# Kernel optimization log

Measured on AMD Instinct MI355X. Metric: run time of the kernel, lower is better.

Reference implementation:

```python
import jax, jax.numpy as jnp
import numpy as np


def setup_inputs() -> dict:
    key = jax.random.key(0)
    k1, k2 = jax.random.split(key)
    qs = jax.random.normal(k1, (64, 32, 128), dtype=jnp.float32)   # (n_queries, n_query_tokens, dim)
    ps = jax.random.normal(k2, (64, 1024, 128), dtype=jnp.float32)  # (n_docs, n_doc_tokens, dim)
    return {"qs": qs, "ps": ps}


def reference(qs, ps):
    # ColBERT MaxSim: for each (query b, doc c), sum over query tokens of the
    # max similarity against all doc tokens.
    # scores[b,c,n,s] = sum_d qs[b,n,d] * ps[c,s,d]
    sim = jnp.einsum('bnd,csd->bcns', qs, ps)  # (n_q, n_d, tok_q, tok_d)
    scores = sim.max(axis=3).sum(axis=2)       # (n_q, n_d)
    return scores
```

## Files before the change

### kernel.cpp

```cpp
#include <hip/hip_runtime.h>
#include <stdint.h>


typedef __bf16 bf16x8 __attribute__((ext_vector_type(8)));
typedef float floatx16 __attribute__((ext_vector_type(16)));

#define QS_N (64u * 32u * 128u)
#define PS_N (64u * 1024u * 128u)

__device__ inline unsigned short f2bf(float f) {
  union { float f; uint32_t u; } x{f};
  uint32_t r = (x.u + 0x7FFFu + ((x.u >> 16) & 1u)) >> 16;
  return (unsigned short)r;
}

__global__ __launch_bounds__(256) void cvt_kernel(const float* __restrict__ qs,
                                                  const float* __restrict__ ps,
                                                  ushort* __restrict__ outb) {
  const int nq4 = QS_N / 4;
  const int n4 = (QS_N + PS_N) / 4;
  int i = blockIdx.x * 256 + threadIdx.x;
  if (i >= n4) return;
  float4 f;
  if (i < nq4) {
    f = ((const float4*)qs)[i];
  } else {
    f = ((const float4*)ps)[i - nq4];
  }
  ushort4 o;
  o.x = f2bf(f.x); o.y = f2bf(f.y); o.z = f2bf(f.z); o.w = f2bf(f.w);
  ((ushort4*)outb)[i] = o;
}

union FragU { uint4 u; bf16x8 v; };

__device__ inline bf16x8 load_frag_bf16(const ushort* p) {
  FragU f;
  f.u = *(const uint4*)p;
  return f.v;
}

__device__ inline bf16x8 load_frag_f32(const float* p) {
  float4 a = *(const float4*)p;
  float4 b = *(const float4*)(p + 4);
  union { ushort s[8]; bf16x8 v; } r;
  r.s[0] = f2bf(a.x); r.s[1] = f2bf(a.y); r.s[2] = f2bf(a.z); r.s[3] = f2bf(a.w);
  r.s[4] = f2bf(b.x); r.s[5] = f2bf(b.y); r.s[6] = f2bf(b.z); r.s[7] = f2bf(b.w);
  return r.v;
}

template <bool PRECVT>
__device__ inline bf16x8 load_a(const void* p, int off) {
  return PRECVT ? load_frag_bf16((const ushort*)p + off)
                : load_frag_f32((const float*)p + off);
}

template <bool PRECVT>
__global__ __launch_bounds__(256) void maxsim_kernel(const void* __restrict__ qsv,
                                                     const void* __restrict__ psv,
                                                     float* __restrict__ out) {
  const int lane = threadIdx.x & 63;
  const int wave = threadIdx.x >> 6;

  const int xcd = blockIdx.x & 7;
  const int slot = blockIdx.x >> 3;
  const int c = xcd * 8 + (slot >> 4);
  const int bg = slot & 15;
  const int row = lane & 31;
  const int koff = (lane >> 5) * 8;
  const int b0 = bg * 4;

  const int pbase = (c * 1024 + wave * 256 + row) * 128 + koff;

  bf16x8 a0[8], a1[8];
#pragma unroll
  for (int k = 0; k < 8; ++k) a0[k] = load_a<PRECVT>(psv, pbase + k * 16);

  bf16x8 qf[4][8];
#pragma unroll
  for (int b = 0; b < 4; ++b)
#pragma unroll
    for (int k = 0; k < 8; ++k)
      qf[b][k] = load_a<PRECVT>(qsv, ((b0 + b) * 32 + row) * 128 + k * 16 + koff);

  float vmax[4];
#pragma unroll
  for (int b = 0; b < 4; ++b) vmax[b] = -3.4e38f;

#pragma unroll 1
  for (int t = 0; t < 8; t += 2) {
#pragma unroll
    for (int k = 0; k < 8; ++k)
      a1[k] = load_a<PRECVT>(psv, pbase + (t + 1) * 4096 + k * 16);
#pragma unroll
    for (int b = 0; b < 4; ++b) {
      floatx16 acc = {0, 0, 0, 0, 0, 0, 0, 0, 0, 0, 0, 0, 0, 0, 0, 0};
#pragma unroll
      for (int k = 0; k < 8; ++k)
        acc = __builtin_amdgcn_mfma_f32_32x32x16_bf16(a0[k], qf[b][k], acc, 0, 0, 0);
      float m0 = fmaxf(fmaxf(fmaxf(acc[0], acc[1]), fmaxf(acc[2], acc[3])),
                       fmaxf(fmaxf(acc[4], acc[5]), fmaxf(acc[6], acc[7])));
      float m1 = fmaxf(fmaxf(fmaxf(acc[8], acc[9]), fmaxf(acc[10], acc[11])),
                       fmaxf(fmaxf(acc[12], acc[13]), fmaxf(acc[14], acc[15])));
      vmax[b] = fmaxf(vmax[b], fmaxf(m0, m1));
    }
    int t2 = t + 2;
    if (t2 > 7) t2 = 0;
#pragma unroll
    for (int k = 0; k < 8; ++k)
      a0[k] = load_a<PRECVT>(psv, pbase + t2 * 4096 + k * 16);
#pragma unroll
    for (int b = 0; b < 4; ++b) {
      floatx16 acc = {0, 0, 0, 0, 0, 0, 0, 0, 0, 0, 0, 0, 0, 0, 0, 0};
#pragma unroll
      for (int k = 0; k < 8; ++k)
        acc = __builtin_amdgcn_mfma_f32_32x32x16_bf16(a1[k], qf[b][k], acc, 0, 0, 0);
      float m0 = fmaxf(fmaxf(fmaxf(acc[0], acc[1]), fmaxf(acc[2], acc[3])),
                       fmaxf(fmaxf(acc[4], acc[5]), fmaxf(acc[6], acc[7])));
      float m1 = fmaxf(fmaxf(fmaxf(acc[8], acc[9]), fmaxf(acc[10], acc[11])),
                       fmaxf(fmaxf(acc[12], acc[13]), fmaxf(acc[14], acc[15])));
      vmax[b] = fmaxf(vmax[b], fmaxf(m0, m1));
    }
  }

#pragma unroll
  for (int b = 0; b < 4; ++b) vmax[b] = fmaxf(vmax[b], __shfl_xor(vmax[b], 32, 64));

  __shared__ float red[4][4][32];
  if (lane < 32) {
#pragma unroll
    for (int b = 0; b < 4; ++b) red[wave][b][lane] = vmax[b];
  }
  __syncthreads();
  if (threadIdx.x < 128) {
    const int b = threadIdx.x >> 5;
    const int n = threadIdx.x & 31;
    float m = fmaxf(fmaxf(red[0][b][n], red[1][b][n]), fmaxf(red[2][b][n], red[3][b][n]));
#pragma unroll
    for (int o = 16; o > 0; o >>= 1) m += __shfl_xor(m, o, 32);
    if (n == 0) out[(b0 + b) * 64 + c] = m;
  }
}

extern "C" void kernel_launch(void* const* d_in, const int* in_sizes, int n_in,
                              void* d_out, int out_size, void* d_ws, size_t ws_size,
                              hipStream_t stream) {
  const float* qs = (const float*)d_in[0];
  const float* ps = (const float*)d_in[1];
  float* out = (float*)d_out;

  const size_t need = (QS_N + PS_N) * sizeof(ushort);

  if (ws_size >= need) {
    ushort* wsb = (ushort*)d_ws;
    const int n4 = (int)((QS_N + PS_N) / 4);
    cvt_kernel<<<(n4 + 255) / 256, 256, 0, stream>>>(qs, ps, wsb);
    maxsim_kernel<true><<<dim3(64 * 16), dim3(256), 0, stream>>>(wsb, wsb + QS_N, out);
  } else {
    maxsim_kernel<false><<<dim3(64 * 16), dim3(256), 0, stream>>>(qs, ps, out);
  }
}
```

Baseline: 129.2 us.

## Stage query fragments in LDS and interleave four independent MFMA accumulators

Query fragments are now loaded cooperatively into shared memory once per block and read from LDS inside the loop, instead of each wave holding all 32 query fragments in registers. The MFMA loop is reordered so four independent accumulator chains run interleaved over k, which hides MFMA dependency latency. This frees many VGPRs, which can raise occupancy, at the cost of repeated LDS reads and a block-wide barrier at the start.

```diff
diff --git a/kernel.cpp b/kernel.cpp
--- a/kernel.cpp
+++ b/kernel.cpp
@@ -55,6 +55,16 @@
                 : load_frag_f32((const float*)p + off);
 }
 
+__device__ inline float rmax16(const floatx16& a) {
+  float m0 = fmaxf(fmaxf(a[0], a[1]), fmaxf(a[2], a[3]));
+  float m1 = fmaxf(fmaxf(a[4], a[5]), fmaxf(a[6], a[7]));
+  float m2 = fmaxf(fmaxf(a[8], a[9]), fmaxf(a[10], a[11]));
+  float m3 = fmaxf(fmaxf(a[12], a[13]), fmaxf(a[14], a[15]));
+  return fmaxf(fmaxf(m0, m1), fmaxf(m2, m3));
+}
+
+#define ZERO16 {0, 0, 0, 0, 0, 0, 0, 0, 0, 0, 0, 0, 0, 0, 0, 0}
+
 template <bool PRECVT>
 __global__ __launch_bounds__(256) void maxsim_kernel(const void* __restrict__ qsv,
                                                      const void* __restrict__ psv,
@@ -66,22 +76,44 @@
   const int slot = blockIdx.x >> 3;
   const int c = xcd * 8 + (slot >> 4);
   const int bg = slot & 15;
+  const int b0 = bg * 4;
   const int row = lane & 31;
   const int koff = (lane >> 5) * 8;
-  const int b0 = bg * 4;
+
+  __shared__ ushort lds_q[4 * 8 * 64 * 8];
+  {
+    uint4* dst = (uint4*)lds_q;
+#pragma unroll
+    for (int i = 0; i < 8; ++i) {
+      const int id = threadIdx.x + i * 256;
+      const int l = id & 63;
+      const int k = (id >> 6) & 7;
+      const int b = id >> 9;
+      const int goff = ((b0 + b) * 32 + (l & 31)) * 128 + k * 16 + (l >> 5) * 8;
+      uint4 v;
+      if (PRECVT) {
+        v = *(const uint4*)((const ushort*)qsv + goff);
+      } else {
+        const float* q = (const float*)qsv + goff;
+        float4 x = *(const float4*)q;
+        float4 y = *(const float4*)(q + 4);
+        union { ushort s[8]; uint4 u; } r;
+        r.s[0] = f2bf(x.x); r.s[1] = f2bf(x.y); r.s[2] = f2bf(x.z); r.s[3] = f2bf(x.w);
+        r.s[4] = f2bf(y.x); r.s[5] = f2bf(y.y); r.s[6] = f2bf(y.z); r.s[7] = f2bf(y.w);
+        v = r.u;
+      }
+      dst[id] = v;
+    }
+  }
+  __syncthreads();
+
+  const ushort* lq = lds_q + lane * 8;
 
   const int pbase = (c * 1024 + wave * 256 + row) * 128 + koff;
 
   bf16x8 a0[8], a1[8];
 #pragma unroll
   for (int k = 0; k < 8; ++k) a0[k] = load_a<PRECVT>(psv, pbase + k * 16);
-
-  bf16x8 qf[4][8];
-#pragma unroll
-  for (int b = 0; b < 4; ++b)
-#pragma unroll
-    for (int k = 0; k < 8; ++k)
-      qf[b][k] = load_a<PRECVT>(qsv, ((b0 + b) * 32 + row) * 128 + k * 16 + koff);
 
   float vmax[4];
 #pragma unroll
@@ -92,34 +124,46 @@
 #pragma unroll
     for (int k = 0; k < 8; ++k)
       a1[k] = load_a<PRECVT>(psv, pbase + (t + 1) * 4096 + k * 16);
-#pragma unroll
-    for (int b = 0; b < 4; ++b) {
-      floatx16 acc = {0, 0, 0, 0, 0, 0, 0, 0, 0, 0, 0, 0, 0, 0, 0, 0};
-#pragma unroll
-      for (int k = 0; k < 8; ++k)
-        acc = __builtin_amdgcn_mfma_f32_32x32x16_bf16(a0[k], qf[b][k], acc, 0, 0, 0);
-      float m0 = fmaxf(fmaxf(fmaxf(acc[0], acc[1]), fmaxf(acc[2], acc[3])),
-                       fmaxf(fmaxf(acc[4], acc[5]), fmaxf(acc[6], acc[7])));
-      float m1 = fmaxf(fmaxf(fmaxf(acc[8], acc[9]), fmaxf(acc[10], acc[11])),
-                       fmaxf(fmaxf(acc[12], acc[13]), fmaxf(acc[14], acc[15])));
-      vmax[b] = fmaxf(vmax[b], fmaxf(m0, m1));
+    {
+      floatx16 acc0 = ZERO16, acc1 = ZERO16, acc2 = ZERO16, acc3 = ZERO16;
+#pragma unroll
+      for (int k = 0; k < 8; ++k) {
+        bf16x8 q0 = *(const bf16x8*)(lq + (0 * 8 + k) * 512);
+        bf16x8 q1 = *(const bf16x8*)(lq + (1 * 8 + k) * 512);
+        bf16x8 q2 = *(const bf16x8*)(lq + (2 * 8 + k) * 512);
+        bf16x8 q3 = *(const bf16x8*)(lq + (3 * 8 + k) * 512);
+        acc0 = __builtin_amdgcn_mfma_f32_32x32x16_bf16(a0[k], q0, acc0, 0, 0, 0);
+        acc1 = __builtin_amdgcn_mfma_f32_32x32x16_bf16(a0[k], q1, acc1, 0, 0, 0);
+        acc2 = __builtin_amdgcn_mfma_f32_32x32x16_bf16(a0[k], q2, acc2, 0, 0, 0);
+        acc3 = __builtin_amdgcn_mfma_f32_32x32x16_bf16(a0[k], q3, acc3, 0, 0, 0);
+      }
+      vmax[0] = fmaxf(vmax[0], rmax16(acc0));
+      vmax[1] = fmaxf(vmax[1], rmax16(acc1));
+      vmax[2] = fmaxf(vmax[2], rmax16(acc2));
+      vmax[3] = fmaxf(vmax[3], rmax16(acc3));
     }
     int t2 = t + 2;
     if (t2 > 7) t2 = 0;
 #pragma unroll
     for (int k = 0; k < 8; ++k)
       a0[k] = load_a<PRECVT>(psv, pbase + t2 * 4096 + k * 16);
-#pragma unroll
-    for (int b = 0; b < 4; ++b) {
-      floatx16 acc = {0, 0, 0, 0, 0, 0, 0, 0, 0, 0, 0, 0, 0, 0, 0, 0};
-#pragma unroll
-      for (int k = 0; k < 8; ++k)
-        acc = __builtin_amdgcn_mfma_f32_32x32x16_bf16(a1[k], qf[b][k], acc, 0, 0, 0);
-      float m0 = fmaxf(fmaxf(fmaxf(acc[0], acc[1]), fmaxf(acc[2], acc[3])),
-                       fmaxf(fmaxf(acc[4], acc[5]), fmaxf(acc[6], acc[7])));
-      float m1 = fmaxf(fmaxf(fmaxf(acc[8], acc[9]), fmaxf(acc[10], acc[11])),
-                       fmaxf(fmaxf(acc[12], acc[13]), fmaxf(acc[14], acc[15])));
-      vmax[b] = fmaxf(vmax[b], fmaxf(m0, m1));
+    {
+      floatx16 acc0 = ZERO16, acc1 = ZERO16, acc2 = ZERO16, acc3 = ZERO16;
+#pragma unroll
+      for (int k = 0; k < 8; ++k) {
+        bf16x8 q0 = *(const bf16x8*)(lq + (0 * 8 + k) * 512);
+        bf16x8 q1 = *(const bf16x8*)(lq + (1 * 8 + k) * 512);
+        bf16x8 q2 = *(const bf16x8*)(lq + (2 * 8 + k) * 512);
+        bf16x8 q3 = *(const bf16x8*)(lq + (3 * 8 + k) * 512);
+        acc0 = __builtin_amdgcn_mfma_f32_32x32x16_bf16(a1[k], q0, acc0, 0, 0, 0);
+        acc1 = __builtin_amdgcn_mfma_f32_32x32x16_bf16(a1[k], q1, acc1, 0, 0, 0);
+        acc2 = __builtin_amdgcn_mfma_f32_32x32x16_bf16(a1[k], q2, acc2, 0, 0, 0);
+        acc3 = __builtin_amdgcn_mfma_f32_32x32x16_bf16(a1[k], q3, acc3, 0, 0, 0);
+      }
+      vmax[0] = fmaxf(vmax[0], rmax16(acc0));
+      vmax[1] = fmaxf(vmax[1], rmax16(acc1));
+      vmax[2] = fmaxf(vmax[2], rmax16(acc2));
+      vmax[3] = fmaxf(vmax[3], rmax16(acc3));
     }
   }
 
```

After: 135.0 us. 4.5% more time.

## Switch MaxSim MFMA tiles from 32x32x16 to 16x16x32 with smaller register footprint

Applied to the files above, without the earlier changes.

Replaces the 32x32x16 bf16 MFMA tiling with 16x16x32 MFMAs. Each wave now processes 16 doc rows per step over 16 steps, and query fragments are split into two 16-row halves. Accumulators shrink from 16 floats to 4 per tile, and launch_bounds now requests 2 blocks per CU, aiming for higher occupancy and better latency hiding. The cost is more MFMA instructions per tile, more shuffle reductions, and an empty asm barrier that pins the query registers.

```diff
diff --git a/kernel.cpp b/kernel.cpp
--- a/kernel.cpp
+++ b/kernel.cpp
@@ -3,7 +3,7 @@
 
 
 typedef __bf16 bf16x8 __attribute__((ext_vector_type(8)));
-typedef float floatx16 __attribute__((ext_vector_type(16)));
+typedef float floatx4 __attribute__((ext_vector_type(4)));
 
 #define QS_N (64u * 32u * 128u)
 #define PS_N (64u * 1024u * 128u)
@@ -34,31 +34,54 @@
 
 union FragU { uint4 u; bf16x8 v; };
 
-__device__ inline bf16x8 load_frag_bf16(const ushort* p) {
-  FragU f;
-  f.u = *(const uint4*)p;
-  return f.v;
-}
-
-__device__ inline bf16x8 load_frag_f32(const float* p) {
-  float4 a = *(const float4*)p;
-  float4 b = *(const float4*)(p + 4);
-  union { ushort s[8]; bf16x8 v; } r;
-  r.s[0] = f2bf(a.x); r.s[1] = f2bf(a.y); r.s[2] = f2bf(a.z); r.s[3] = f2bf(a.w);
-  r.s[4] = f2bf(b.x); r.s[5] = f2bf(b.y); r.s[6] = f2bf(b.z); r.s[7] = f2bf(b.w);
-  return r.v;
+__device__ inline bf16x8 as_frag(uint4 u) {
+  FragU x;
+  x.u = u;
+  return x.v;
 }
 
 template <bool PRECVT>
-__device__ inline bf16x8 load_a(const void* p, int off) {
-  return PRECVT ? load_frag_bf16((const ushort*)p + off)
-                : load_frag_f32((const float*)p + off);
+__device__ inline uint4 load16(const void* p, int off) {
+  if (PRECVT) {
+    return *(const uint4*)((const ushort*)p + off);
+  } else {
+    const float* q = (const float*)p + off;
+    float4 x = *(const float4*)q;
+    float4 y = *(const float4*)(q + 4);
+    union { ushort s[8]; uint4 u; } r;
+    r.s[0] = f2bf(x.x); r.s[1] = f2bf(x.y); r.s[2] = f2bf(x.z); r.s[3] = f2bf(x.w);
+    r.s[4] = f2bf(y.x); r.s[5] = f2bf(y.y); r.s[6] = f2bf(y.z); r.s[7] = f2bf(y.w);
+    return r.u;
+  }
 }
 
+#define ZERO4 {0, 0, 0, 0}
+
+#define TILE_COMPUTE(ABUF)                                                      \
+  {                                                                             \
+    floatx4 acc[4][2];                                                          \
+    _Pragma("unroll") for (int b = 0; b < 4; ++b)                               \
+      _Pragma("unroll") for (int h = 0; h < 2; ++h)                             \
+        acc[b][h] = (floatx4)ZERO4;                                             \
+    _Pragma("unroll") for (int k2 = 0; k2 < 4; ++k2) {                          \
+      bf16x8 af = as_frag(ABUF[k2]);                                            \
+      _Pragma("unroll") for (int b = 0; b < 4; ++b)                             \
+        _Pragma("unroll") for (int h = 0; h < 2; ++h)                           \
+          acc[b][h] = __builtin_amdgcn_mfma_f32_16x16x32_bf16(                  \
+              af, as_frag(qfr[b][h][k2]), acc[b][h], 0, 0, 0);                  \
+    }                                                                           \
+    _Pragma("unroll") for (int b = 0; b < 4; ++b)                               \
+      _Pragma("unroll") for (int h = 0; h < 2; ++h) {                           \
+        float m = fmaxf(fmaxf(acc[b][h][0], acc[b][h][1]),                      \
+                        fmaxf(acc[b][h][2], acc[b][h][3]));                     \
+        vmax[b][h] = fmaxf(vmax[b][h], m);                                      \
+      }                                                                         \
+  }
+
 template <bool PRECVT>
-__global__ __launch_bounds__(256) void maxsim_kernel(const void* __restrict__ qsv,
-                                                     const void* __restrict__ psv,
-                                                     float* __restrict__ out) {
+__global__ __launch_bounds__(256, 2) void maxsim_kernel(const void* __restrict__ qsv,
+                                                        const void* __restrict__ psv,
+                                                        float* __restrict__ out) {
   const int lane = threadIdx.x & 63;
   const int wave = threadIdx.x >> 6;
 
@@ -66,70 +89,68 @@
   const int slot = blockIdx.x >> 3;
   const int c = xcd * 8 + (slot >> 4);
   const int bg = slot & 15;
-  const int row = lane & 31;
-  const int koff = (lane >> 5) * 8;
   const int b0 = bg * 4;
 
-  const int pbase = (c * 1024 + wave * 256 + row) * 128 + koff;
+  const int idx16 = lane & 15;
+  const int koff = (lane >> 4) * 8;
 
-  bf16x8 a0[8], a1[8];
-#pragma unroll
-  for (int k = 0; k < 8; ++k) a0[k] = load_a<PRECVT>(psv, pbase + k * 16);
-
-  bf16x8 qf[4][8];
+  uint4 qfr[4][2][4];
 #pragma unroll
   for (int b = 0; b < 4; ++b)
 #pragma unroll
-    for (int k = 0; k < 8; ++k)
-      qf[b][k] = load_a<PRECVT>(qsv, ((b0 + b) * 32 + row) * 128 + k * 16 + koff);
+    for (int h = 0; h < 2; ++h)
+#pragma unroll
+      for (int k2 = 0; k2 < 4; ++k2) {
+        const int goff = ((b0 + b) * 32 + h * 16 + idx16) * 128 + k2 * 32 + koff;
+        uint4 v = load16<PRECVT>(qsv, goff);
+        asm volatile("" : "+v"(v.x), "+v"(v.y), "+v"(v.z), "+v"(v.w));
+        qfr[b][h][k2] = v;
+      }
 
-  float vmax[4];
+  const int pbase = (c * 1024 + wave * 256 + idx16) * 128 + koff;
+
+  uint4 a0[4], a1[4];
 #pragma unroll
-  for (int b = 0; b < 4; ++b) vmax[b] = -3.4e38f;
+  for (int k2 = 0; k2 < 4; ++k2) a0[k2] = load16<PRECVT>(psv, pbase + k2 * 32);
+
+  float vmax[4][2];
+#pragma unroll
+  for (int b = 0; b < 4; ++b) {
+    vmax[b][0] = -3.4e38f;
+    vmax[b][1] = -3.4e38f;
+  }
 
 #pragma unroll 1
-  for (int t = 0; t < 8; t += 2) {
+  for (int t = 0; t < 16; t += 2) {
 #pragma unroll
-    for (int k = 0; k < 8; ++k)
-      a1[k] = load_a<PRECVT>(psv, pbase + (t + 1) * 4096 + k * 16);
+    for (int k2 = 0; k2 < 4; ++k2)
+      a1[k2] = load16<PRECVT>(psv, pbase + (t + 1) * 2048 + k2 * 32);
+    TILE_COMPUTE(a0)
+    int t2 = t + 2;
+    if (t2 > 15) t2 = 0;
 #pragma unroll
-    for (int b = 0; b < 4; ++b) {
-      floatx16 acc = {0, 0, 0, 0, 0, 0, 0, 0, 0, 0, 0, 0, 0, 0, 0, 0};
-#pragma unroll
-      for (int k = 0; k < 8; ++k)
-        acc = __builtin_amdgcn_mfma_f32_32x32x16_bf16(a0[k], qf[b][k], acc, 0, 0, 0);
-      float m0 = fmaxf(fmaxf(fmaxf(acc[0], acc[1]), fmaxf(acc[2], acc[3])),
-                       fmaxf(fmaxf(acc[4], acc[5]), fmaxf(acc[6], acc[7])));
-      float m1 = fmaxf(fmaxf(fmaxf(acc[8], acc[9]), fmaxf(acc[10], acc[11])),
-                       fmaxf(fmaxf(acc[12], acc[13]), fmaxf(acc[14], acc[15])));
-      vmax[b] = fmaxf(vmax[b], fmaxf(m0, m1));
-    }
-    int t2 = t + 2;
-    if (t2 > 7) t2 = 0;
-#pragma unroll
-    for (int k = 0; k < 8; ++k)
-      a0[k] = load_a<PRECVT>(psv, pbase + t2 * 4096 + k * 16);
-#pragma unroll
-    for (int b = 0; b < 4; ++b) {
-      floatx16 acc = {0, 0, 0, 0, 0, 0, 0, 0, 0, 0, 0, 0, 0, 0, 0, 0};
-#pragma unroll
-      for (int k = 0; k < 8; ++k)
-        acc = __builtin_amdgcn_mfma_f32_32x32x16_bf16(a1[k], qf[b][k], acc, 0, 0, 0);
-      float m0 = fmaxf(fmaxf(fmaxf(acc[0], acc[1]), fmaxf(acc[2], acc[3])),
-                       fmaxf(fmaxf(acc[4], acc[5]), fmaxf(acc[6], acc[7])));
-      float m1 = fmaxf(fmaxf(fmaxf(acc[8], acc[9]), fmaxf(acc[10], acc[11])),
-                       fmaxf(fmaxf(acc[12], acc[13]), fmaxf(acc[14], acc[15])));
-      vmax[b] = fmaxf(vmax[b], fmaxf(m0, m1));
-    }
+    for (int k2 = 0; k2 < 4; ++k2)
+      a0[k2] = load16<PRECVT>(psv, pbase + t2 * 2048 + k2 * 32);
+    TILE_COMPUTE(a1)
   }
 
 #pragma unroll
-  for (int b = 0; b < 4; ++b) vmax[b] = fmaxf(vmax[b], __shfl_xor(vmax[b], 32, 64));
+  for (int b = 0; b < 4; ++b)
+#pragma unroll
+    for (int h = 0; h < 2; ++h) {
+      float v = vmax[b][h];
+      v = fmaxf(v, __shfl_xor(v, 16, 64));
+      v = fmaxf(v, __shfl_xor(v, 32, 64));
+      vmax[b][h] = v;
+    }
 
   __shared__ float red[4][4][32];
-  if (lane < 32) {
+  if (lane < 16) {
 #pragma unroll
-    for (int b = 0; b < 4; ++b) red[wave][b][lane] = vmax[b];
+    for (int b = 0; b < 4; ++b) {
+      red[wave][b][lane] = vmax[b][0];
+      red[wave][b][16 + lane] = vmax[b][1];
+    }
   }
   __syncthreads();
   if (threadIdx.x < 128) {
```

New measurement: 128.2 us. About the same (-0.8%).
